# Performance work log

Measured on AMD Instinct MI355X. Metric: run time of the kernel, lower is better.

Reference implementation:

```python
import jax, jax.numpy as jnp
import numpy as np

B, N, H, W, C = 512, 16, 84, 84, 3
CNN_OUT, ATTN, GH, HEADS, POS, A_DIM = 256, 64, 128, 2, 3, 3
IN_GAT = CNN_OUT + POS  # 259
FLAT = 64 * 16 * 16     # conv output flat dim for 84x84 input


def setup_inputs() -> dict:
    key = jax.random.key(0)
    ks = jax.random.split(key, 16)
    s = 0.05
    return dict(
        cam=jax.random.uniform(ks[0], (B, H, W, C), jnp.float32),
        pos=jax.random.normal(ks[1], (B, POS), jnp.float32),
        team_pos=jax.random.normal(ks[2], (B, N, POS), jnp.float32) * 10.0,
        agent_idx=jax.random.randint(ks[3], (B,), 0, N),
        W1=jax.random.normal(ks[4], (32, C, 8, 8), jnp.float32) * s, b1=jnp.zeros((32,), jnp.float32),
        W2=jax.random.normal(ks[5], (64, 32, 4, 4), jnp.float32) * s, b2=jnp.zeros((64,), jnp.float32),
        W3=jax.random.normal(ks[6], (64, 64, 3, 3), jnp.float32) * s, b3=jnp.zeros((64,), jnp.float32),
        Wp=jax.random.normal(ks[7], (FLAT, CNN_OUT), jnp.float32) * 0.01, bp=jnp.zeros((CNN_OUT,), jnp.float32),
        Wid=jax.random.normal(ks[8], (1, ATTN), jnp.float32) * s, bid=jnp.zeros((ATTN,), jnp.float32),
        Wg=jax.random.normal(ks[9], (IN_GAT, HEADS * GH), jnp.float32) * s,
        a_src=jax.random.normal(ks[10], (HEADS, GH), jnp.float32) * s,
        a_dst=jax.random.normal(ks[11], (HEADS, GH), jnp.float32) * s,
        Wh1=jax.random.normal(ks[12], (HEADS * GH + ATTN, 256), jnp.float32) * s, bh1=jnp.zeros((256,), jnp.float32),
        Wh2=jax.random.normal(ks[13], (256, 2 * A_DIM), jnp.float32) * s, bh2=jnp.zeros((2 * A_DIM,), jnp.float32),
    )


def _conv(x, w, b, stride):
    y = jax.lax.conv_general_dilated(x, w, (stride, stride), 'VALID',
                                     dimension_numbers=('NCHW', 'OIHW', 'NCHW'))
    return jax.nn.relu(y + b[None, :, None, None])


def reference(cam, pos, team_pos, agent_idx, W1, b1, W2, b2, W3, b3, Wp, bp,
              Wid, bid, Wg, a_src, a_dst, Wh1, bh1, Wh2, bh2):
    # CNN encoder (NHWC -> NCHW)
    x = jnp.transpose(cam, (0, 3, 1, 2))
    x = _conv(x, W1, b1, 2)   # [B,32,39,39]
    x = _conv(x, W2, b2, 2)   # [B,64,18,18]
    x = _conv(x, W3, b3, 1)   # [B,64,16,16]
    cam_feat = jax.nn.relu(x.reshape(x.shape[0], -1) @ Wp + bp)  # [B,256]

    # per-node features: broadcast ego cam feat + relative team positions
    rel_pos = team_pos - pos[:, None, :]                                     # [B,N,3]
    node_feats = jnp.concatenate(
        [jnp.broadcast_to(cam_feat[:, None, :], (B, N, CNN_OUT)), rel_pos], axis=-1)  # [B,N,259]

    # adjacency: within 100m, no self-loops, self-loop added for isolated nodes
    dist = jnp.linalg.norm(team_pos[:, :, None, :] - team_pos[:, None, :, :], axis=-1)  # [B,N,N]
    eye = jnp.eye(N, dtype=node_feats.dtype)
    adj = (dist < 100.0).astype(node_feats.dtype) * (1.0 - eye)
    need_self = (adj.sum(axis=2) == 0).astype(adj.dtype)                     # [B,N]
    adj = adj + eye[None] * need_self[..., None]

    # dense multi-head GAT layer
    hN = (node_feats @ Wg).reshape(B, N, HEADS, GH)                          # [B,N,H,D]
    src = jnp.einsum('bnhd,hd->bnh', hN, a_src)
    dst = jnp.einsum('bnhd,hd->bnh', hN, a_dst)
    e = jax.nn.leaky_relu(src[:, :, None, :] + dst[:, None, :, :], 0.2)      # [B,i,j,H]
    e = jnp.where(adj[..., None] > 0, e, -1e9)
    alpha = jax.nn.softmax(e, axis=2)
    h = jnp.einsum('bijh,bjhd->bihd', alpha, hN).reshape(B, N, HEADS * GH)   # [B,N,256]
    h = jax.nn.elu(h)
    h = jnp.nan_to_num(h, nan=0.0, posinf=0.0, neginf=0.0)

    # agent-id embedding, fuse, gather own node, policy head
    id_emb = jax.nn.relu(agent_idx.astype(jnp.float32)[:, None] @ Wid + bid)  # [B,64]
    fused = jnp.concatenate([h, jnp.broadcast_to(id_emb[:, None, :], (B, N, ATTN))], axis=-1)  # [B,N,320]
    agent_feat = fused[jnp.arange(B), agent_idx]                             # [B,320]
    z = jax.nn.relu(agent_feat @ Wh1 + bh1)
    logits = z @ Wh2 + bh2                                                    # [B,6]
    return logits
```

## Files before the change

kernel.cpp:

```cpp
#include <hip/hip_runtime.h>


typedef __attribute__((ext_vector_type(8))) short bf16x8;
typedef __attribute__((ext_vector_type(4))) float f32x4;

union U4 { uint4 v; unsigned int u[4]; bf16x8 h; };

__device__ __forceinline__ unsigned short f2bf(float x) {
    unsigned int u = __float_as_uint(x);
    return (unsigned short)((u + 0x7FFFu + ((u >> 16) & 1u)) >> 16);
}
__device__ __forceinline__ unsigned int pack2(float lo, float hi) {
    return (unsigned int)f2bf(lo) | ((unsigned int)f2bf(hi) << 16);
}
__device__ __forceinline__ bf16x8 loadA(const unsigned int* __restrict__ W, int k8, int M, int oc) {
    U4 r; r.v = *(const uint4*)(W + (((size_t)k8 * M + oc) << 2));
    return r.h;
}
__device__ __forceinline__ bf16x8 loadB(const unsigned int* __restrict__ p, size_t BC) {
    U4 r; r.u[0] = p[0]; r.u[1] = p[BC]; r.u[2] = p[2 * BC]; r.u[3] = p[3 * BC];
    return r.h;
}
#define MFMA(a, b, c) __builtin_amdgcn_mfma_f32_16x16x32_bf16((a), (b), (c), 0, 0, 0)

__global__ __launch_bounds__(256) void prepack(
    const float* __restrict__ W1, const float* __restrict__ W2,
    const float* __restrict__ W3, const float* __restrict__ Wp,
    unsigned int* __restrict__ W1t, unsigned int* __restrict__ W2t,
    unsigned int* __restrict__ W3t, unsigned int* __restrict__ Wpt)
{
    int i = blockIdx.x * 256 + threadIdx.x;
    if (i < 3072) {
        int j2 = i & 3, oc = (i >> 2) & 31, k8 = i >> 7;
        int c = k8 >> 3, kh = k8 & 7, kw = 2 * j2;
        const float* s = W1 + ((oc * 3 + c) * 8 + kh) * 8;
        W1t[i] = pack2(s[kw], s[kw + 1]);
    } else if (i < 3072 + 16384) {
        int j = i - 3072;
        int j2 = j & 3, oc = (j >> 2) & 63, k8 = j >> 8;
        int tap = k8 >> 2, ic = (k8 & 3) * 8 + 2 * j2;
        int kh = tap >> 2, kw = tap & 3;
        float a = W2[((oc * 32 + ic) * 4 + kh) * 4 + kw];
        float b = W2[((oc * 32 + ic + 1) * 4 + kh) * 4 + kw];
        W2t[j] = pack2(a, b);
    } else if (i < 3072 + 16384 + 18432) {
        int j = i - 3072 - 16384;
        int j2 = j & 3, oc = (j >> 2) & 63, k8 = j >> 8;
        int tap = k8 >> 3, ic = (k8 & 7) * 8 + 2 * j2;
        int kh = tap / 3, kw = tap % 3;
        float a = W3[((oc * 64 + ic) * 3 + kh) * 3 + kw];
        float b = W3[((oc * 64 + ic + 1) * 3 + kh) * 3 + kw];
        W3t[j] = pack2(a, b);
    } else {
        int j = i - 3072 - 16384 - 18432;
        if (j < 2097152) {
            int j2 = j & 3, n = (j >> 2) & 255, k8 = j >> 10;
            int s3 = k8 >> 3, oc = (k8 & 7) * 8 + 2 * j2;
            float a = Wp[(size_t)(oc * 256 + s3) * 256 + n];
            float b = Wp[(size_t)((oc + 1) * 256 + s3) * 256 + n];
            Wpt[j] = pack2(a, b);
        }
    }
}

__global__ __launch_bounds__(256) void transpose_cam(
    const float* __restrict__ cam, unsigned int* __restrict__ camt, int b0, int BC)
{
    __shared__ float lds[32][253];
    int yy = blockIdx.x;
    int bb = blockIdx.y * 32;
    int t = threadIdx.x;
    for (int f = t; f < 8064; f += 256) {
        int b = f / 252, p = f - b * 252;
        lds[b][p] = cam[(size_t)(b0 + bb + b) * 21168 + yy * 252 + p];
    }
    __syncthreads();
    for (int g = t; g < 4032; g += 256) {
        int b = g & 31, q = g >> 5;
        int c = q / 42, x2 = q - c * 42;
        unsigned int v = pack2(lds[b][6 * x2 + c], lds[b][6 * x2 + 3 + c]);
        camt[(size_t)((c * 84 + yy) * 42 + x2) * BC + bb + b] = v;
    }
}

__global__ __launch_bounds__(256) void conv1_mfma(
    const unsigned int* __restrict__ in32, const unsigned int* __restrict__ Wt,
    const float* __restrict__ bias, unsigned int* __restrict__ out32, int BC)
{
    int s = blockIdx.x; int oh = s / 39, ow = s - oh * 39;
    int wv = threadIdx.x >> 6, l = threadIdx.x & 63;
    int lg = l >> 4, lc = l & 15;
    const size_t sBC = (size_t)BC;
    size_t bcol = (size_t)blockIdx.y * 128 + wv * 32 + lc;
    f32x4 acc[2][2] = {};
    int ybase = 2 * oh;
    #pragma unroll
    for (int sp = 0; sp < 3; sp++) {
        const int s0 = 2 * sp, s1 = s0 + 1;
        bf16x8 A0[2], A1[2], B0[2], B1[2];
        #pragma unroll
        for (int m = 0; m < 2; m++) {
            A0[m] = loadA(Wt, s0 * 4 + lg, 32, m * 16 + lc);
            A1[m] = loadA(Wt, s1 * 4 + lg, 32, m * 16 + lc);
        }
        const unsigned int* p0 = in32 + (size_t)((sp * 84 + ybase + lg) * 42 + ow) * sBC + bcol;
        const unsigned int* p1 = in32 + (size_t)((sp * 84 + ybase + 4 + lg) * 42 + ow) * sBC + bcol;
        B0[0] = loadB(p0, sBC); B0[1] = loadB(p0 + 16, sBC);
        B1[0] = loadB(p1, sBC); B1[1] = loadB(p1 + 16, sBC);
        #pragma unroll
        for (int m = 0; m < 2; m++) {
            acc[m][0] = MFMA(A0[m], B0[0], acc[m][0]);
            acc[m][1] = MFMA(A0[m], B0[1], acc[m][1]);
            acc[m][0] = MFMA(A1[m], B1[0], acc[m][0]);
            acc[m][1] = MFMA(A1[m], B1[1], acc[m][1]);
        }
    }
    #pragma unroll
    for (int m = 0; m < 2; m++) {
        float4 bv = *(const float4*)(bias + m * 16 + lg * 4);
        #pragma unroll
        for (int g = 0; g < 2; g++) {
            f32x4 a = acc[m][g];
            unsigned int u0 = pack2(fmaxf(a.x + bv.x, 0.f), fmaxf(a.y + bv.y, 0.f));
            unsigned int u1 = pack2(fmaxf(a.z + bv.z, 0.f), fmaxf(a.w + bv.w, 0.f));
            size_t o = (size_t)(s * 16 + m * 8 + lg * 2) * sBC
                     + (size_t)blockIdx.y * 128 + wv * 32 + g * 16 + lc;
            out32[o] = u0; out32[o + sBC] = u1;
        }
    }
}

__global__ __launch_bounds__(256) void conv2_mfma(
    const unsigned int* __restrict__ in32, const unsigned int* __restrict__ Wt,
    const float* __restrict__ bias, unsigned int* __restrict__ out32, int BC)
{
    int s = blockIdx.x; int oh = s / 18, ow = s - oh * 18;
    int wv = threadIdx.x >> 6, l = threadIdx.x & 63;
    int lg = l >> 4, lc = l & 15;
    const size_t sBC = (size_t)BC;
    size_t bcol = (size_t)blockIdx.y * 128 + wv * 32 + lc;
    f32x4 acc[4][2] = {};
    int ybase = 2 * oh, xbase = 2 * ow;
    #pragma unroll
    for (int sp = 0; sp < 8; sp++) {
        const int s0 = 2 * sp, s1 = s0 + 1;
        bf16x8 A0[4], A1[4], B0[2], B1[2];
        #pragma unroll
        for (int m = 0; m < 4; m++) {
            A0[m] = loadA(Wt, s0 * 4 + lg, 64, m * 16 + lc);
            A1[m] = loadA(Wt, s1 * 4 + lg, 64, m * 16 + lc);
        }
        {
            const int kh = s0 >> 2, kw = s0 & 3;
            const unsigned int* p = in32
                + (size_t)((((ybase + kh) * 39 + xbase + kw) * 16) + lg * 4) * sBC + bcol;
            B0[0] = loadB(p, sBC); B0[1] = loadB(p + 16, sBC);
        }
        {
            const int kh = s1 >> 2, kw = s1 & 3;
            const unsigned int* p = in32
                + (size_t)((((ybase + kh) * 39 + xbase + kw) * 16) + lg * 4) * sBC + bcol;
            B1[0] = loadB(p, sBC); B1[1] = loadB(p + 16, sBC);
        }
        #pragma unroll
        for (int m = 0; m < 4; m++) {
            acc[m][0] = MFMA(A0[m], B0[0], acc[m][0]);
            acc[m][1] = MFMA(A0[m], B0[1], acc[m][1]);
        }
        #pragma unroll
        for (int m = 0; m < 4; m++) {
            acc[m][0] = MFMA(A1[m], B1[0], acc[m][0]);
            acc[m][1] = MFMA(A1[m], B1[1], acc[m][1]);
        }
    }
    #pragma unroll
    for (int m = 0; m < 4; m++) {
        float4 bv = *(const float4*)(bias + m * 16 + lg * 4);
        #pragma unroll
        for (int g = 0; g < 2; g++) {
            f32x4 a = acc[m][g];
            unsigned int u0 = pack2(fmaxf(a.x + bv.x, 0.f), fmaxf(a.y + bv.y, 0.f));
            unsigned int u1 = pack2(fmaxf(a.z + bv.z, 0.f), fmaxf(a.w + bv.w, 0.f));
            size_t o = (size_t)(s * 32 + m * 8 + lg * 2) * sBC
                     + (size_t)blockIdx.y * 128 + wv * 32 + g * 16 + lc;
            out32[o] = u0; out32[o + sBC] = u1;
        }
    }
}

__global__ __launch_bounds__(256) void conv3_mfma(
    const unsigned int* __restrict__ in32, const unsigned int* __restrict__ Wt,
    const float* __restrict__ bias, unsigned int* __restrict__ out32, int BC)
{
    int s = blockIdx.x; int oh = s >> 4, ow = s & 15;
    int wv = threadIdx.x >> 6, l = threadIdx.x & 63;
    int lg = l >> 4, lc = l & 15;
    const size_t sBC = (size_t)BC;
    size_t bcol = (size_t)blockIdx.y * 128 + wv * 32 + lc;
    f32x4 acc[4][2] = {};
    #pragma unroll
    for (int sp = 0; sp < 9; sp++) {
        const int s0 = 2 * sp, s1 = s0 + 1;
        const int kh = sp / 3, kw = sp - kh * 3;
        bf16x8 A0[4], A1[4], B0[2], B1[2];
        #pragma unroll
        for (int m = 0; m < 4; m++) {
            A0[m] = loadA(Wt, s0 * 4 + lg, 64, m * 16 + lc);
            A1[m] = loadA(Wt, s1 * 4 + lg, 64, m * 16 + lc);
        }
        const unsigned int* pb = in32
            + (size_t)((((oh + kh) * 18 + ow + kw) * 32)) * sBC;
        const unsigned int* p0 = pb + (size_t)(lg * 4) * sBC + bcol;
        const unsigned int* p1 = pb + (size_t)((4 + lg) * 4) * sBC + bcol;
        B0[0] = loadB(p0, sBC); B0[1] = loadB(p0 + 16, sBC);
        B1[0] = loadB(p1, sBC); B1[1] = loadB(p1 + 16, sBC);
        #pragma unroll
        for (int m = 0; m < 4; m++) {
            acc[m][0] = MFMA(A0[m], B0[0], acc[m][0]);
            acc[m][1] = MFMA(A0[m], B0[1], acc[m][1]);
        }
        #pragma unroll
        for (int m = 0; m < 4; m++) {
            acc[m][0] = MFMA(A1[m], B1[0], acc[m][0]);
            acc[m][1] = MFMA(A1[m], B1[1], acc[m][1]);
        }
    }
    #pragma unroll
    for (int m = 0; m < 4; m++) {
        float4 bv = *(const float4*)(bias + m * 16 + lg * 4);
        #pragma unroll
        for (int g = 0; g < 2; g++) {
            f32x4 a = acc[m][g];
            unsigned int u0 = pack2(fmaxf(a.x + bv.x, 0.f), fmaxf(a.y + bv.y, 0.f));
            unsigned int u1 = pack2(fmaxf(a.z + bv.z, 0.f), fmaxf(a.w + bv.w, 0.f));
            size_t o = (size_t)(s * 32 + m * 8 + lg * 2) * sBC
                     + (size_t)blockIdx.y * 128 + wv * 32 + g * 16 + lc;
            out32[o] = u0; out32[o + sBC] = u1;
        }
    }
}

__global__ __launch_bounds__(256) void proj_mfma(
    const unsigned int* __restrict__ x3, const unsigned int* __restrict__ Wpt,
    float* __restrict__ partial, int BC)
{
    int mq = blockIdx.x;
    int kseg = blockIdx.z;
    int wv = threadIdx.x >> 6, l = threadIdx.x & 63;
    int lg = l >> 4, lc = l & 15;
    const size_t sBC = (size_t)BC;
    size_t bcol = (size_t)blockIdx.y * 128 + wv * 32 + lc;
    f32x4 acc[4][2] = {};
    #pragma unroll
    for (int sp = 0; sp < 8; sp++) {
        const int s0 = 2 * sp, s1 = s0 + 1;
        const int s3 = kseg * 8 + sp;
        bf16x8 A0[4], A1[4], B0[2], B1[2];
        #pragma unroll
        for (int m = 0; m < 4; m++) {
            A0[m] = loadA(Wpt, kseg * 64 + s0 * 4 + lg, 256, mq * 64 + m * 16 + lc);
            A1[m] = loadA(Wpt, kseg * 64 + s1 * 4 + lg, 256, mq * 64 + m * 16 + lc);
        }
        const unsigned int* pb = x3 + (size_t)(s3 * 32) * sBC;
        const unsigned int* p0 = pb + (size_t)(lg * 4) * sBC + bcol;
        const unsigned int* p1 = pb + (size_t)((4 + lg) * 4) * sBC + bcol;
        B0[0] = loadB(p0, sBC); B0[1] = loadB(p0 + 16, sBC);
        B1[0] = loadB(p1, sBC); B1[1] = loadB(p1 + 16, sBC);
        #pragma unroll
        for (int m = 0; m < 4; m++) {
            acc[m][0] = MFMA(A0[m], B0[0], acc[m][0]);
            acc[m][1] = MFMA(A0[m], B0[1], acc[m][1]);
        }
        #pragma unroll
        for (int m = 0; m < 4; m++) {
            acc[m][0] = MFMA(A1[m], B1[0], acc[m][0]);
            acc[m][1] = MFMA(A1[m], B1[1], acc[m][1]);
        }
    }
    #pragma unroll
    for (int m = 0; m < 4; m++) {
        #pragma unroll
        for (int g = 0; g < 2; g++) {
            f32x4 a = acc[m][g];
            float* pp = partial
                + (size_t)(kseg * 256 + mq * 64 + m * 16 + lg * 4) * sBC
                + (size_t)blockIdx.y * 128 + wv * 32 + g * 16 + lc;
            pp[0] = a.x; pp[sBC] = a.y; pp[2 * sBC] = a.z; pp[3 * sBC] = a.w;
        }
    }
}

__global__ __launch_bounds__(256) void reduce_k(
    const float* __restrict__ partial, const float* __restrict__ bp,
    float* __restrict__ camfeat, int b0, int BC, int bcShift)
{
    int i = blockIdx.x * 256 + threadIdx.x;
    int bl = i & (BC - 1);
    int n = i >> bcShift;
    float s = 0.f;
    for (int seg = 0; seg < 32; seg++)
        s += partial[((size_t)(seg * 256 + n) << bcShift) + bl];
    camfeat[(size_t)(b0 + bl) * 256 + n] = fmaxf(s + bp[n], 0.f);
}

__global__ __launch_bounds__(256) void gat_head(
    const float* __restrict__ camfeat, const float* __restrict__ pos,
    const float* __restrict__ tpos, const int* __restrict__ aidx,
    const float* __restrict__ Wg, const float* __restrict__ asrc, const float* __restrict__ adst,
    const float* __restrict__ Wid, const float* __restrict__ bid,
    const float* __restrict__ Wh1, const float* __restrict__ bh1,
    const float* __restrict__ Wh2, const float* __restrict__ bh2,
    float* __restrict__ out)
{
    int b = blockIdx.x, t = threadIdx.x;
    __shared__ float cf[256];
    __shared__ float hN[16][256];
    __shared__ float srcv[16][2], dstv[16][2];
    __shared__ float alpha[16][2];
    __shared__ float af[320];
    __shared__ float zz[256];
    __shared__ unsigned int adjm_s;

    int ai = aidx[b];
    cf[t] = camfeat[b * 256 + t];
    __syncthreads();

    float basev = 0.f;
    for (int k = 0; k < 256; k++) basev += cf[k] * Wg[k * 256 + t];

    float rw0 = Wg[256 * 256 + t], rw1 = Wg[257 * 256 + t], rw2 = Wg[258 * 256 + t];
    float px = pos[b * 3 + 0], py = pos[b * 3 + 1], pz = pos[b * 3 + 2];
    for (int n = 0; n < 16; n++) {
        float r0 = tpos[(b * 16 + n) * 3 + 0] - px;
        float r1 = tpos[(b * 16 + n) * 3 + 1] - py;
        float r2 = tpos[(b * 16 + n) * 3 + 2] - pz;
        hN[n][t] = basev + r0 * rw0 + r1 * rw1 + r2 * rw2;
    }

    if (t < 64) {
        bool on = false;
        if (t < 16 && t != ai) {
            float dx = tpos[(b * 16 + ai) * 3 + 0] - tpos[(b * 16 + t) * 3 + 0];
            float dy = tpos[(b * 16 + ai) * 3 + 1] - tpos[(b * 16 + t) * 3 + 1];
            float dz = tpos[(b * 16 + ai) * 3 + 2] - tpos[(b * 16 + t) * 3 + 2];
            on = (dx * dx + dy * dy + dz * dz) < 10000.0f;
        }
        unsigned long long m = __ballot(on);
        if (t == 0) adjm_s = (m == 0ull) ? (1u << ai) : (unsigned int)m;
    }
    __syncthreads();

    {
        int p = t >> 3, sub = t & 7;
        int j = p >> 1, h = p & 1;
        float s1 = 0.f, s2 = 0.f;
        #pragma unroll
        for (int dd = 0; dd < 16; dd++) {
            int d = h * 128 + sub * 16 + dd;
            float v = hN[j][d];
            s1 += v * asrc[d];
            s2 += v * adst[d];
        }
        s1 += __shfl_xor(s1, 1); s1 += __shfl_xor(s1, 2); s1 += __shfl_xor(s1, 4);
        s2 += __shfl_xor(s2, 1); s2 += __shfl_xor(s2, 2); s2 += __shfl_xor(s2, 4);
        if (sub == 0) { srcv[j][h] = s1; dstv[j][h] = s2; }
    }
    __syncthreads();

    if (t < 32) {
        int j = t & 15, h = t >> 4;
        unsigned int am = adjm_s;
        float e = srcv[ai][h] + dstv[j][h];
        e = (e > 0.f) ? e : 0.2f * e;
        e = ((am >> j) & 1u) ? e : -1e9f;
        float mx = e;
        mx = fmaxf(mx, __shfl_xor(mx, 1));
        mx = fmaxf(mx, __shfl_xor(mx, 2));
        mx = fmaxf(mx, __shfl_xor(mx, 4));
        mx = fmaxf(mx, __shfl_xor(mx, 8));
        float ex = __expf(e - mx);
        float sm = ex;
        sm += __shfl_xor(sm, 1); sm += __shfl_xor(sm, 2);
        sm += __shfl_xor(sm, 4); sm += __shfl_xor(sm, 8);
        alpha[j][h] = ex / sm;
    }
    __syncthreads();

    {
        int h = t >> 7;
        float o = 0.f;
        #pragma unroll
        for (int j = 0; j < 16; j++) o += alpha[j][h] * hN[j][t];
        o = (o > 0.f) ? o : (__expf(o) - 1.f);
        af[t] = o;
    }
    if (t < 64) {
        float v = (float)ai * Wid[t] + bid[t];
        af[256 + t] = fmaxf(v, 0.f);
    }
    __syncthreads();

    float zv = bh1[t];
    for (int k = 0; k < 320; k++) zv += af[k] * Wh1[k * 256 + t];
    zz[t] = fmaxf(zv, 0.f);
    __syncthreads();

    if (t < 6) {
        float lv = bh2[t];
        for (int k = 0; k < 256; k++) lv += zz[k] * Wh2[k * 6 + t];
        out[b * 6 + t] = lv;
    }
}

extern "C" void kernel_launch(void* const* d_in, const int* in_sizes, int n_in,
                              void* d_out, int out_size, void* d_ws, size_t ws_size,
                              hipStream_t stream)
{
    const float* cam  = (const float*)d_in[0];
    const float* pos  = (const float*)d_in[1];
    const float* tpos = (const float*)d_in[2];
    const int*   aidx = (const int*)d_in[3];
    const float* W1   = (const float*)d_in[4];
    const float* b1   = (const float*)d_in[5];
    const float* W2   = (const float*)d_in[6];
    const float* b2   = (const float*)d_in[7];
    const float* W3   = (const float*)d_in[8];
    const float* b3   = (const float*)d_in[9];
    const float* Wp   = (const float*)d_in[10];
    const float* bp   = (const float*)d_in[11];
    const float* Wid  = (const float*)d_in[12];
    const float* bid  = (const float*)d_in[13];
    const float* Wg   = (const float*)d_in[14];
    const float* asrc = (const float*)d_in[15];
    const float* adst = (const float*)d_in[16];
    const float* Wh1  = (const float*)d_in[17];
    const float* bh1  = (const float*)d_in[18];
    const float* Wh2  = (const float*)d_in[19];
    const float* bh2  = (const float*)d_in[20];
    float* out = (float*)d_out;

    int BC = 128;
    {
        const int cands[3] = {512, 256, 128};
        for (int idx = 0; idx < 3; idx++) {
            size_t need = ((size_t)51304 * cands[idx] + 2266112) * 4;
            if (need <= ws_size) { BC = cands[idx]; break; }
        }
    }
    int bcShift = (BC == 512) ? 9 : (BC == 256) ? 8 : 7;

    unsigned int* ws32 = (unsigned int*)d_ws;
    unsigned int* RA  = ws32;
    unsigned int* RB  = RA + (size_t)10584 * BC;
    unsigned int* RC  = RB + (size_t)24336 * BC;
    float*        RD  = (float*)(RC + (size_t)8192 * BC);
    unsigned int* W1t = (unsigned int*)(RD + (size_t)8192 * BC);
    unsigned int* W2t = W1t + 3072;
    unsigned int* W3t = W2t + 16384;
    unsigned int* Wpt = W3t + 18432;
    float* camfeat    = (float*)(Wpt + 2097152);

    prepack<<<8340, 256, 0, stream>>>(W1, W2, W3, Wp, W1t, W2t, W3t, Wpt);

    for (int b0 = 0; b0 < 512; b0 += BC) {
        transpose_cam<<<dim3(84, BC / 32), 256, 0, stream>>>(cam, RA, b0, BC);
        conv1_mfma<<<dim3(1521, BC / 128), 256, 0, stream>>>(RA, W1t, b1, RB, BC);
        conv2_mfma<<<dim3(324, BC / 128), 256, 0, stream>>>(RB, W2t, b2, RA, BC);
        conv3_mfma<<<dim3(256, BC / 128), 256, 0, stream>>>(RA, W3t, b3, RC, BC);
        proj_mfma<<<dim3(4, BC / 128, 32), 256, 0, stream>>>(RC, Wpt, RD, BC);
        reduce_k<<<BC, 256, 0, stream>>>(RD, bp, camfeat, b0, BC, bcShift);
    }
    gat_head<<<512, 256, 0, stream>>>(camfeat, pos, tpos, aidx, Wg, asrc, adst,
                                      Wid, bid, Wh1, bh1, Wh2, bh2, out);
}
```

Baseline: 164.2 us.

## Move GAT projection and head MLP to batched MFMA GEMMs, add XCD swizzle

Splits the per-sample gat_head kernel into a batched bf16 MFMA GEMM for the camera-feature part of the GAT projection, a per-sample attention kernel, a batched MFMA GEMM for the first head layer, and a small logits kernel. This replaces the per-block scalar loops that re-read Wg and Wh1 for every sample. The conv and projection kernels also move to a 1D grid with an XCD-aware block-index swizzle to improve L2 locality across chiplets. In exchange it adds bf16 rounding on the GAT and head inputs, more kernel launches, and extra workspace.

```diff
diff --git a/kernel.cpp b/kernel.cpp
--- a/kernel.cpp
+++ b/kernel.cpp
@@ -23,11 +23,19 @@
 }
 #define MFMA(a, b, c) __builtin_amdgcn_mfma_f32_16x16x32_bf16((a), (b), (c), 0, 0, 0)
 
+__device__ __forceinline__ int xcd_swz(int L, int nwg) {
+    int q = nwg >> 3, r = nwg & 7;
+    int x = L & 7, i = L >> 3;
+    return (x < r ? x * (q + 1) : r * (q + 1) + (x - r) * q) + i;
+}
+
 __global__ __launch_bounds__(256) void prepack(
     const float* __restrict__ W1, const float* __restrict__ W2,
     const float* __restrict__ W3, const float* __restrict__ Wp,
+    const float* __restrict__ Wg, const float* __restrict__ Wh1,
     unsigned int* __restrict__ W1t, unsigned int* __restrict__ W2t,
-    unsigned int* __restrict__ W3t, unsigned int* __restrict__ Wpt)
+    unsigned int* __restrict__ W3t, unsigned int* __restrict__ Wpt,
+    unsigned int* __restrict__ Wgt, unsigned int* __restrict__ Wh1t)
 {
     int i = blockIdx.x * 256 + threadIdx.x;
     if (i < 3072) {
@@ -35,7 +43,7 @@
         int c = k8 >> 3, kh = k8 & 7, kw = 2 * j2;
         const float* s = W1 + ((oc * 3 + c) * 8 + kh) * 8;
         W1t[i] = pack2(s[kw], s[kw + 1]);
-    } else if (i < 3072 + 16384) {
+    } else if (i < 19456) {
         int j = i - 3072;
         int j2 = j & 3, oc = (j >> 2) & 63, k8 = j >> 8;
         int tap = k8 >> 2, ic = (k8 & 3) * 8 + 2 * j2;
@@ -43,23 +51,31 @@
         float a = W2[((oc * 32 + ic) * 4 + kh) * 4 + kw];
         float b = W2[((oc * 32 + ic + 1) * 4 + kh) * 4 + kw];
         W2t[j] = pack2(a, b);
-    } else if (i < 3072 + 16384 + 18432) {
-        int j = i - 3072 - 16384;
+    } else if (i < 37888) {
+        int j = i - 19456;
         int j2 = j & 3, oc = (j >> 2) & 63, k8 = j >> 8;
         int tap = k8 >> 3, ic = (k8 & 7) * 8 + 2 * j2;
         int kh = tap / 3, kw = tap % 3;
         float a = W3[((oc * 64 + ic) * 3 + kh) * 3 + kw];
         float b = W3[((oc * 64 + ic + 1) * 3 + kh) * 3 + kw];
         W3t[j] = pack2(a, b);
-    } else {
-        int j = i - 3072 - 16384 - 18432;
-        if (j < 2097152) {
-            int j2 = j & 3, n = (j >> 2) & 255, k8 = j >> 10;
-            int s3 = k8 >> 3, oc = (k8 & 7) * 8 + 2 * j2;
-            float a = Wp[(size_t)(oc * 256 + s3) * 256 + n];
-            float b = Wp[(size_t)((oc + 1) * 256 + s3) * 256 + n];
-            Wpt[j] = pack2(a, b);
-        }
+    } else if (i < 2135040) {
+        int j = i - 37888;
+        int j2 = j & 3, n = (j >> 2) & 255, k8 = j >> 10;
+        int s3 = k8 >> 3, oc = (k8 & 7) * 8 + 2 * j2;
+        float a = Wp[(size_t)(oc * 256 + s3) * 256 + n];
+        float b = Wp[(size_t)((oc + 1) * 256 + s3) * 256 + n];
+        Wpt[j] = pack2(a, b);
+    } else if (i < 2167808) {
+        int j = i - 2135040;
+        int j2 = j & 3, m = (j >> 2) & 255, k8 = j >> 10;
+        int k = k8 * 8 + 2 * j2;
+        Wgt[j] = pack2(Wg[k * 256 + m], Wg[(k + 1) * 256 + m]);
+    } else if (i < 2208768) {
+        int j = i - 2167808;
+        int j2 = j & 3, m = (j >> 2) & 255, k8 = j >> 10;
+        int k = k8 * 8 + 2 * j2;
+        Wh1t[j] = pack2(Wh1[k * 256 + m], Wh1[(k + 1) * 256 + m]);
     }
 }
 
@@ -85,13 +101,16 @@
 
 __global__ __launch_bounds__(256) void conv1_mfma(
     const unsigned int* __restrict__ in32, const unsigned int* __restrict__ Wt,
-    const float* __restrict__ bias, unsigned int* __restrict__ out32, int BC)
-{
-    int s = blockIdx.x; int oh = s / 39, ow = s - oh * 39;
+    const float* __restrict__ bias, unsigned int* __restrict__ out32, int BC, int bqShift)
+{
+    int wgid = xcd_swz(blockIdx.x, gridDim.x);
+    int bq = wgid & ((1 << bqShift) - 1);
+    int s = wgid >> bqShift;
+    int oh = s / 39, ow = s - oh * 39;
     int wv = threadIdx.x >> 6, l = threadIdx.x & 63;
     int lg = l >> 4, lc = l & 15;
     const size_t sBC = (size_t)BC;
-    size_t bcol = (size_t)blockIdx.y * 128 + wv * 32 + lc;
+    size_t bcol = (size_t)bq * 128 + wv * 32 + lc;
     f32x4 acc[2][2] = {};
     int ybase = 2 * oh;
     #pragma unroll
@@ -124,7 +143,7 @@
             unsigned int u0 = pack2(fmaxf(a.x + bv.x, 0.f), fmaxf(a.y + bv.y, 0.f));
             unsigned int u1 = pack2(fmaxf(a.z + bv.z, 0.f), fmaxf(a.w + bv.w, 0.f));
             size_t o = (size_t)(s * 16 + m * 8 + lg * 2) * sBC
-                     + (size_t)blockIdx.y * 128 + wv * 32 + g * 16 + lc;
+                     + (size_t)bq * 128 + wv * 32 + g * 16 + lc;
             out32[o] = u0; out32[o + sBC] = u1;
         }
     }
@@ -132,13 +151,16 @@
 
 __global__ __launch_bounds__(256) void conv2_mfma(
     const unsigned int* __restrict__ in32, const unsigned int* __restrict__ Wt,
-    const float* __restrict__ bias, unsigned int* __restrict__ out32, int BC)
-{
-    int s = blockIdx.x; int oh = s / 18, ow = s - oh * 18;
+    const float* __restrict__ bias, unsigned int* __restrict__ out32, int BC, int bqShift)
+{
+    int wgid = xcd_swz(blockIdx.x, gridDim.x);
+    int bq = wgid & ((1 << bqShift) - 1);
+    int s = wgid >> bqShift;
+    int oh = s / 18, ow = s - oh * 18;
     int wv = threadIdx.x >> 6, l = threadIdx.x & 63;
     int lg = l >> 4, lc = l & 15;
     const size_t sBC = (size_t)BC;
-    size_t bcol = (size_t)blockIdx.y * 128 + wv * 32 + lc;
+    size_t bcol = (size_t)bq * 128 + wv * 32 + lc;
     f32x4 acc[4][2] = {};
     int ybase = 2 * oh, xbase = 2 * ow;
     #pragma unroll
@@ -182,7 +204,7 @@
             unsigned int u0 = pack2(fmaxf(a.x + bv.x, 0.f), fmaxf(a.y + bv.y, 0.f));
             unsigned int u1 = pack2(fmaxf(a.z + bv.z, 0.f), fmaxf(a.w + bv.w, 0.f));
             size_t o = (size_t)(s * 32 + m * 8 + lg * 2) * sBC
-                     + (size_t)blockIdx.y * 128 + wv * 32 + g * 16 + lc;
+                     + (size_t)bq * 128 + wv * 32 + g * 16 + lc;
             out32[o] = u0; out32[o + sBC] = u1;
         }
     }
@@ -190,13 +212,16 @@
 
 __global__ __launch_bounds__(256) void conv3_mfma(
     const unsigned int* __restrict__ in32, const unsigned int* __restrict__ Wt,
-    const float* __restrict__ bias, unsigned int* __restrict__ out32, int BC)
-{
-    int s = blockIdx.x; int oh = s >> 4, ow = s & 15;
+    const float* __restrict__ bias, unsigned int* __restrict__ out32, int BC, int bqShift)
+{
+    int wgid = xcd_swz(blockIdx.x, gridDim.x);
+    int bq = wgid & ((1 << bqShift) - 1);
+    int s = wgid >> bqShift;
+    int oh = s >> 4, ow = s & 15;
     int wv = threadIdx.x >> 6, l = threadIdx.x & 63;
     int lg = l >> 4, lc = l & 15;
     const size_t sBC = (size_t)BC;
-    size_t bcol = (size_t)blockIdx.y * 128 + wv * 32 + lc;
+    size_t bcol = (size_t)bq * 128 + wv * 32 + lc;
     f32x4 acc[4][2] = {};
     #pragma unroll
     for (int sp = 0; sp < 9; sp++) {
@@ -208,8 +233,7 @@
             A0[m] = loadA(Wt, s0 * 4 + lg, 64, m * 16 + lc);
             A1[m] = loadA(Wt, s1 * 4 + lg, 64, m * 16 + lc);
         }
-        const unsigned int* pb = in32
-            + (size_t)((((oh + kh) * 18 + ow + kw) * 32)) * sBC;
+        const unsigned int* pb = in32 + (size_t)((((oh + kh) * 18 + ow + kw) * 32)) * sBC;
         const unsigned int* p0 = pb + (size_t)(lg * 4) * sBC + bcol;
         const unsigned int* p1 = pb + (size_t)((4 + lg) * 4) * sBC + bcol;
         B0[0] = loadB(p0, sBC); B0[1] = loadB(p0 + 16, sBC);
@@ -234,7 +258,7 @@
             unsigned int u0 = pack2(fmaxf(a.x + bv.x, 0.f), fmaxf(a.y + bv.y, 0.f));
             unsigned int u1 = pack2(fmaxf(a.z + bv.z, 0.f), fmaxf(a.w + bv.w, 0.f));
             size_t o = (size_t)(s * 32 + m * 8 + lg * 2) * sBC
-                     + (size_t)blockIdx.y * 128 + wv * 32 + g * 16 + lc;
+                     + (size_t)bq * 128 + wv * 32 + g * 16 + lc;
             out32[o] = u0; out32[o + sBC] = u1;
         }
     }
@@ -242,14 +266,17 @@
 
 __global__ __launch_bounds__(256) void proj_mfma(
     const unsigned int* __restrict__ x3, const unsigned int* __restrict__ Wpt,
-    float* __restrict__ partial, int BC)
-{
-    int mq = blockIdx.x;
-    int kseg = blockIdx.z;
+    float* __restrict__ partial, int BC, int bqShift)
+{
+    int wgid = xcd_swz(blockIdx.x, gridDim.x);
+    int bq = wgid & ((1 << bqShift) - 1);
+    int rem = wgid >> bqShift;
+    int mq = rem & 3;
+    int kseg = rem >> 2;
     int wv = threadIdx.x >> 6, l = threadIdx.x & 63;
     int lg = l >> 4, lc = l & 15;
     const size_t sBC = (size_t)BC;
-    size_t bcol = (size_t)blockIdx.y * 128 + wv * 32 + lc;
+    size_t bcol = (size_t)bq * 128 + wv * 32 + lc;
     f32x4 acc[4][2] = {};
     #pragma unroll
     for (int sp = 0; sp < 8; sp++) {
@@ -284,7 +311,7 @@
             f32x4 a = acc[m][g];
             float* pp = partial
                 + (size_t)(kseg * 256 + mq * 64 + m * 16 + lg * 4) * sBC
-                + (size_t)blockIdx.y * 128 + wv * 32 + g * 16 + lc;
+                + (size_t)bq * 128 + wv * 32 + g * 16 + lc;
             pp[0] = a.x; pp[sBC] = a.y; pp[2 * sBC] = a.z; pp[3 * sBC] = a.w;
         }
     }
@@ -292,43 +319,82 @@
 
 __global__ __launch_bounds__(256) void reduce_k(
     const float* __restrict__ partial, const float* __restrict__ bp,
-    float* __restrict__ camfeat, int b0, int BC, int bcShift)
+    unsigned int* __restrict__ cf16, int b0, int BC, int bcShift)
 {
     int i = blockIdx.x * 256 + threadIdx.x;
     int bl = i & (BC - 1);
-    int n = i >> bcShift;
-    float s = 0.f;
-    for (int seg = 0; seg < 32; seg++)
-        s += partial[((size_t)(seg * 256 + n) << bcShift) + bl];
-    camfeat[(size_t)(b0 + bl) * 256 + n] = fmaxf(s + bp[n], 0.f);
-}
-
-__global__ __launch_bounds__(256) void gat_head(
-    const float* __restrict__ camfeat, const float* __restrict__ pos,
+    int q = i >> bcShift;
+    float s0 = 0.f, s1 = 0.f;
+    int n0 = 2 * q;
+    for (int seg = 0; seg < 32; seg++) {
+        s0 += partial[((size_t)(seg * 256 + n0) << bcShift) + bl];
+        s1 += partial[((size_t)(seg * 256 + n0 + 1) << bcShift) + bl];
+    }
+    float v0 = fmaxf(s0 + bp[n0], 0.f);
+    float v1 = fmaxf(s1 + bp[n0 + 1], 0.f);
+    cf16[(size_t)q * 512 + b0 + bl] = pack2(v0, v1);
+}
+
+__global__ __launch_bounds__(64) void gat_prep(
+    const unsigned int* __restrict__ cf16, const unsigned int* __restrict__ Wgt,
+    float* __restrict__ hNb)
+{
+    int mq = blockIdx.x, bq = blockIdx.y;
+    int l = threadIdx.x, lg = l >> 4, lc = l & 15;
+    size_t bcol = (size_t)bq * 32 + lc;
+    f32x4 acc[4][2] = {};
+    #pragma unroll
+    for (int sp = 0; sp < 4; sp++) {
+        const int s0 = 2 * sp, s1 = s0 + 1;
+        bf16x8 A0[4], A1[4], B0[2], B1[2];
+        #pragma unroll
+        for (int m = 0; m < 4; m++) {
+            A0[m] = loadA(Wgt, s0 * 4 + lg, 256, mq * 64 + m * 16 + lc);
+            A1[m] = loadA(Wgt, s1 * 4 + lg, 256, mq * 64 + m * 16 + lc);
+        }
+        const unsigned int* p0 = cf16 + (size_t)(sp * 32 + lg * 4) * 512 + bcol;
+        const unsigned int* p1 = p0 + (size_t)16 * 512;
+        B0[0] = loadB(p0, 512); B0[1] = loadB(p0 + 16, 512);
+        B1[0] = loadB(p1, 512); B1[1] = loadB(p1 + 16, 512);
+        #pragma unroll
+        for (int m = 0; m < 4; m++) {
+            acc[m][0] = MFMA(A0[m], B0[0], acc[m][0]);
+            acc[m][1] = MFMA(A0[m], B0[1], acc[m][1]);
+        }
+        #pragma unroll
+        for (int m = 0; m < 4; m++) {
+            acc[m][0] = MFMA(A1[m], B1[0], acc[m][0]);
+            acc[m][1] = MFMA(A1[m], B1[1], acc[m][1]);
+        }
+    }
+    #pragma unroll
+    for (int m = 0; m < 4; m++) {
+        #pragma unroll
+        for (int g = 0; g < 2; g++) {
+            size_t b = (size_t)bq * 32 + g * 16 + lc;
+            int row0 = mq * 64 + m * 16 + lg * 4;
+            *(f32x4*)(hNb + b * 256 + row0) = acc[m][g];
+        }
+    }
+}
+
+__global__ __launch_bounds__(256) void gat_mid(
+    const float* __restrict__ hNb, const float* __restrict__ pos,
     const float* __restrict__ tpos, const int* __restrict__ aidx,
     const float* __restrict__ Wg, const float* __restrict__ asrc, const float* __restrict__ adst,
     const float* __restrict__ Wid, const float* __restrict__ bid,
-    const float* __restrict__ Wh1, const float* __restrict__ bh1,
-    const float* __restrict__ Wh2, const float* __restrict__ bh2,
-    float* __restrict__ out)
+    unsigned int* __restrict__ af16)
 {
     int b = blockIdx.x, t = threadIdx.x;
-    __shared__ float cf[256];
     __shared__ float hN[16][256];
     __shared__ float srcv[16][2], dstv[16][2];
     __shared__ float alpha[16][2];
     __shared__ float af[320];
-    __shared__ float zz[256];
     __shared__ unsigned int adjm_s;
 
     int ai = aidx[b];
-    cf[t] = camfeat[b * 256 + t];
-    __syncthreads();
-
-    float basev = 0.f;
-    for (int k = 0; k < 256; k++) basev += cf[k] * Wg[k * 256 + t];
-
-    float rw0 = Wg[256 * 256 + t], rw1 = Wg[257 * 256 + t], rw2 = Wg[258 * 256 + t];
+    float basev = hNb[(size_t)b * 256 + t];
+    float rw0 = Wg[65536 + t], rw1 = Wg[65792 + t], rw2 = Wg[66048 + t];
     float px = pos[b * 3 + 0], py = pos[b * 3 + 1], pz = pos[b * 3 + 2];
     for (int n = 0; n < 16; n++) {
         float r0 = tpos[(b * 16 + n) * 3 + 0] - px;
@@ -400,16 +466,77 @@
     }
     __syncthreads();
 
-    float zv = bh1[t];
-    for (int k = 0; k < 320; k++) zv += af[k] * Wh1[k * 256 + t];
-    zz[t] = fmaxf(zv, 0.f);
+    if (t < 160) af16[(size_t)t * 512 + b] = pack2(af[2 * t], af[2 * t + 1]);
+}
+
+__global__ __launch_bounds__(64) void head_mfma(
+    const unsigned int* __restrict__ af16, const unsigned int* __restrict__ Wh1t,
+    const float* __restrict__ bh1, float* __restrict__ zf)
+{
+    int mq = blockIdx.x, bq = blockIdx.y;
+    int l = threadIdx.x, lg = l >> 4, lc = l & 15;
+    size_t bcol = (size_t)bq * 32 + lc;
+    f32x4 acc[4][2] = {};
+    #pragma unroll
+    for (int sp = 0; sp < 5; sp++) {
+        const int s0 = 2 * sp, s1 = s0 + 1;
+        bf16x8 A0[4], A1[4], B0[2], B1[2];
+        #pragma unroll
+        for (int m = 0; m < 4; m++) {
+            A0[m] = loadA(Wh1t, s0 * 4 + lg, 256, mq * 64 + m * 16 + lc);
+            A1[m] = loadA(Wh1t, s1 * 4 + lg, 256, mq * 64 + m * 16 + lc);
+        }
+        const unsigned int* p0 = af16 + (size_t)(sp * 32 + lg * 4) * 512 + bcol;
+        const unsigned int* p1 = p0 + (size_t)16 * 512;
+        B0[0] = loadB(p0, 512); B0[1] = loadB(p0 + 16, 512);
+        B1[0] = loadB(p1, 512); B1[1] = loadB(p1 + 16, 512);
+        #pragma unroll
+        for (int m = 0; m < 4; m++) {
+            acc[m][0] = MFMA(A0[m], B0[0], acc[m][0]);
+            acc[m][1] = MFMA(A0[m], B0[1], acc[m][1]);
+        }
+        #pragma unroll
+        for (int m = 0; m < 4; m++) {
+            acc[m][0] = MFMA(A1[m], B1[0], acc[m][0]);
+            acc[m][1] = MFMA(A1[m], B1[1], acc[m][1]);
+        }
+    }
+    #pragma unroll
+    for (int m = 0; m < 4; m++) {
+        int row0 = mq * 64 + m * 16 + lg * 4;
+        float4 bv = *(const float4*)(bh1 + row0);
+        #pragma unroll
+        for (int g = 0; g < 2; g++) {
+            f32x4 a = acc[m][g];
+            size_t b = (size_t)bq * 32 + g * 16 + lc;
+            float* pp = zf + (size_t)row0 * 512 + b;
+            pp[0]        = fmaxf(a.x + bv.x, 0.f);
+            pp[512]      = fmaxf(a.y + bv.y, 0.f);
+            pp[2 * 512]  = fmaxf(a.z + bv.z, 0.f);
+            pp[3 * 512]  = fmaxf(a.w + bv.w, 0.f);
+        }
+    }
+}
+
+__global__ __launch_bounds__(256) void logits_k(
+    const float* __restrict__ zf, const float* __restrict__ Wh2,
+    const float* __restrict__ bh2, float* __restrict__ out)
+{
+    __shared__ float Ws[1536];
+    int t = threadIdx.x;
+    int b = blockIdx.x * 256 + t;
+    for (int f = t; f < 1536; f += 256) Ws[f] = Wh2[f];
     __syncthreads();
-
-    if (t < 6) {
-        float lv = bh2[t];
-        for (int k = 0; k < 256; k++) lv += zz[k] * Wh2[k * 6 + t];
-        out[b * 6 + t] = lv;
-    }
+    float acc[6];
+    #pragma unroll
+    for (int j = 0; j < 6; j++) acc[j] = bh2[j];
+    for (int k = 0; k < 256; k++) {
+        float zv = zf[(size_t)k * 512 + b];
+        #pragma unroll
+        for (int j = 0; j < 6; j++) acc[j] += zv * Ws[k * 6 + j];
+    }
+    #pragma unroll
+    for (int j = 0; j < 6; j++) out[b * 6 + j] = acc[j];
 }
 
 extern "C" void kernel_launch(void* const* d_in, const int* in_sizes, int n_in,
@@ -443,11 +570,13 @@
     {
         const int cands[3] = {512, 256, 128};
         for (int idx = 0; idx < 3; idx++) {
-            size_t need = ((size_t)51304 * cands[idx] + 2266112) * 4;
+            size_t need = ((size_t)51304 * cands[idx] + 2618368) * 4;
             if (need <= ws_size) { BC = cands[idx]; break; }
         }
     }
     int bcShift = (BC == 512) ? 9 : (BC == 256) ? 8 : 7;
+    int nbq = BC >> 7;
+    int bqShift = (BC == 512) ? 2 : (BC == 256) ? 1 : 0;
 
     unsigned int* ws32 = (unsigned int*)d_ws;
     unsigned int* RA  = ws32;
@@ -455,21 +584,30 @@
     unsigned int* RC  = RB + (size_t)24336 * BC;
     float*        RD  = (float*)(RC + (size_t)8192 * BC);
     unsigned int* W1t = (unsigned int*)(RD + (size_t)8192 * BC);
-    unsigned int* W2t = W1t + 3072;
-    unsigned int* W3t = W2t + 16384;
-    unsigned int* Wpt = W3t + 18432;
-    float* camfeat    = (float*)(Wpt + 2097152);
-
-    prepack<<<8340, 256, 0, stream>>>(W1, W2, W3, Wp, W1t, W2t, W3t, Wpt);
+    unsigned int* W2t  = W1t + 3072;
+    unsigned int* W3t  = W2t + 16384;
+    unsigned int* Wpt  = W3t + 18432;
+    unsigned int* Wgt  = Wpt + 2097152;
+    unsigned int* Wh1t = Wgt + 32768;
+    unsigned int* cf16 = Wh1t + 40960;
+    float*        hNb  = (float*)(cf16 + 65536);
+    unsigned int* af16 = (unsigned int*)(hNb + 131072);
+    float*        zf   = (float*)(af16 + 81920);
+
+    prepack<<<8628, 256, 0, stream>>>(W1, W2, W3, Wp, Wg, Wh1,
+                                      W1t, W2t, W3t, Wpt, Wgt, Wh1t);
 
     for (int b0 = 0; b0 < 512; b0 += BC) {
         transpose_cam<<<dim3(84, BC / 32), 256, 0, stream>>>(cam, RA, b0, BC);
-        conv1_mfma<<<dim3(1521, BC / 128), 256, 0, stream>>>(RA, W1t, b1, RB, BC);
-        conv2_mfma<<<dim3(324, BC / 128), 256, 0, stream>>>(RB, W2t, b2, RA, BC);
-        conv3_mfma<<<dim3(256, BC / 128), 256, 0, stream>>>(RA, W3t, b3, RC, BC);
-        proj_mfma<<<dim3(4, BC / 128, 32), 256, 0, stream>>>(RC, Wpt, RD, BC);
-        reduce_k<<<BC, 256, 0, stream>>>(RD, bp, camfeat, b0, BC, bcShift);
-    }
-    gat_head<<<512, 256, 0, stream>>>(camfeat, pos, tpos, aidx, Wg, asrc, adst,
-                                      Wid, bid, Wh1, bh1, Wh2, bh2, out);
-}
+        conv1_mfma<<<1521 * nbq, 256, 0, stream>>>(RA, W1t, b1, RB, BC, bqShift);
+        conv2_mfma<<<324 * nbq, 256, 0, stream>>>(RB, W2t, b2, RA, BC, bqShift);
+        conv3_mfma<<<256 * nbq, 256, 0, stream>>>(RA, W3t, b3, RC, BC, bqShift);
+        proj_mfma<<<128 * nbq, 256, 0, stream>>>(RC, Wpt, RD, BC, bqShift);
+        reduce_k<<<BC / 2, 256, 0, stream>>>(RD, bp, cf16, b0, BC, bcShift);
+    }
+    gat_prep<<<dim3(4, 16), 64, 0, stream>>>(cf16, Wgt, hNb);
+    gat_mid<<<512, 256, 0, stream>>>(hNb, pos, tpos, aidx, Wg, asrc, adst,
+                                     Wid, bid, af16);
+    head_mfma<<<dim3(4, 16), 64, 0, stream>>>(af16, Wh1t, bh1, zf);
+    logits_k<<<2, 256, 0, stream>>>(zf, Wh2, bh2, out);
+}
```

New measurement: 163.5 us. No clear change (-0.5%).
